# Performance work log

Hardware: AMD Instinct MI355X
Metric: run time of the kernel (lower is better)

Reference implementation:

```python
import jax, jax.numpy as jnp
import numpy as np

L, N, E = 2048, 2, 1024
H = 16
INNER = 1024
D = INNER // H  # head dim = 64
SCALE = D ** -0.5


def setup_inputs() -> dict:
    key = jax.random.key(0)
    k1, k2, k3, k4, k5 = jax.random.split(key, 5)
    return {
        "query": jax.random.normal(k1, (L, N, E), dtype=jnp.float32),
        "qkv_proj": jax.random.normal(k2, (3 * INNER, E), dtype=jnp.float32) * 0.02,
        "qkv_bias": jax.random.normal(k3, (3 * INNER,), dtype=jnp.float32) * 0.02,
        "out_proj": jax.random.normal(k4, (E, INNER), dtype=jnp.float32) * 0.02,
        "out_bias": jax.random.normal(k5, (E,), dtype=jnp.float32) * 0.02,
    }


def reference(query, qkv_proj, qkv_bias, out_proj, out_bias):
    # qkv combined projection: [L, N, 3*inner]
    qkv = jnp.einsum('lne,fe->lnf', query, qkv_proj) + qkv_bias
    # torch code views [L, N, 3*inner] as [L, N, inner, 3]: q/k/v interleaved
    qkv = qkv.reshape(L, N, INNER, 3)
    q, k, v = qkv[..., 0], qkv[..., 1], qkv[..., 2]  # each [L, N, inner]
    # [L, N*H, D] -> [N*H, L, D] (batched over batch*heads)
    q = q.reshape(L, N * H, D).transpose(1, 0, 2)
    k = k.reshape(L, N * H, D).transpose(1, 0, 2)
    v = v.reshape(L, N * H, D).transpose(1, 0, 2)
    # scores [N*H, L, L], scaled
    attn = SCALE * jnp.einsum('bld,bmd->blm', q, k)
    attn = jax.nn.softmax(attn, axis=-1)  # dropout_p = 0.0
    out = jnp.einsum('blm,bmd->bld', attn, v)  # [N*H, L, D]
    out = out.transpose(1, 0, 2).reshape(L, N, INNER)
    # output projection + bias
    return jnp.einsum('lni,ei->lne', out, out_proj) + out_bias
```

## Files before the change

### kernel.cpp

```cpp
#include <hip/hip_runtime.h>
#include <stdint.h>

#define SCALE 0.125f
#define LOG2E 1.44269504088896340736f
#define QK_SCALE (SCALE * LOG2E)

typedef __bf16 bf16x8 __attribute__((ext_vector_type(8)));
typedef float f32x4 __attribute__((ext_vector_type(4)));
typedef float f32x16 __attribute__((ext_vector_type(16)));
typedef unsigned u32x4 __attribute__((ext_vector_type(4)));

__device__ __forceinline__ ushort f2bf(float x) {
    union { float f; unsigned u; } v; v.f = x;
    unsigned r = v.u + 0x7FFFu + ((v.u >> 16) & 1u);
    return (ushort)(r >> 16);
}

__device__ __forceinline__ void gld_lds16(const void* g, void* l) {
    __builtin_amdgcn_global_load_lds(
        reinterpret_cast<const unsigned __attribute__((address_space(1)))*>(
            reinterpret_cast<uintptr_t>(g)),
        reinterpret_cast<unsigned __attribute__((address_space(3)))*>(
            (unsigned)reinterpret_cast<uintptr_t>(l)),
        16, 0, 0);
}

__global__ __launch_bounds__(256) void cast_fused(const float* __restrict__ s0,
                                                  const float* __restrict__ s1,
                                                  const float* __restrict__ s2,
                                                  ushort* __restrict__ d0,
                                                  ushort* __restrict__ d1,
                                                  ushort* __restrict__ d2) {
    int i = blockIdx.x * 256 + threadIdx.x;
    const float* src; ushort* dst; int idx;
    if (i < 1048576)            { src = s0; dst = d0; idx = i; }
    else if (i < 1048576 + 786432) { src = s1; dst = d1; idx = i - 1048576; }
    else                        { src = s2; dst = d2; idx = i - (1048576 + 786432); }
    float4 v = ((const float4*)src)[idx];
    ushort4 o;
    o.x = f2bf(v.x); o.y = f2bf(v.y); o.z = f2bf(v.z); o.w = f2bf(v.w);
    ((ushort4*)dst)[idx] = o;
}

__global__ __launch_bounds__(256, 3) void gemm_qkv(
    const ushort* __restrict__ A, const ushort* __restrict__ B,
    const float* __restrict__ bias,
    ushort* __restrict__ qh, ushort* __restrict__ kh, ushort* __restrict__ vT)
{
    __shared__ ushort As[128][64];
    __shared__ ushort Bs[128][64];
    const int tid = threadIdx.x;
    const int lane = tid & 63, wave = tid >> 6;
    const int wr = (wave >> 1) * 64, wc = (wave & 1) * 64;
    const int lr = lane & 15, lg = lane >> 4;
    const int swz = (lr & 7) << 4;
    const int sl = lane >> 3;
    const int scol = ((lane & 7) ^ sl) * 8;
    const int rowBase = blockIdx.y * 128;
    const int which = blockIdx.x >> 3;
    const int i0 = (blockIdx.x & 7) * 128;

    f32x4 acc[4][4] = {};
    for (int k0 = 0; k0 < 1024; k0 += 64) {
        __syncthreads();
        int s0 = wave * 4;
#pragma unroll
        for (int i = 0; i < 4; ++i) {
            int s = s0 + i;
            int r = s * 8 + sl;
            gld_lds16(A + (size_t)(rowBase + r) * 1024 + k0 + scol, &As[s * 8][0]);
            gld_lds16(B + (size_t)(3 * (i0 + r) + which) * 1024 + k0 + scol, &Bs[s * 8][0]);
        }
        __syncthreads();
#pragma unroll
        for (int kk = 0; kk < 2; ++kk) {
            bf16x8 af[4], bfr[4];
#pragma unroll
            for (int m = 0; m < 4; ++m)
                af[m] = *(const bf16x8*)((const char*)As + (wr + m * 16 + lr) * 128 + ((kk * 64 + lg * 16) ^ swz));
#pragma unroll
            for (int n = 0; n < 4; ++n)
                bfr[n] = *(const bf16x8*)((const char*)Bs + (wc + n * 16 + lr) * 128 + ((kk * 64 + lg * 16) ^ swz));
#pragma unroll
            for (int m = 0; m < 4; ++m)
#pragma unroll
                for (int n = 0; n < 4; ++n)
                    acc[m][n] = __builtin_amdgcn_mfma_f32_16x16x32_bf16(af[m], bfr[n], acc[m][n], 0, 0, 0);
        }
    }
#pragma unroll
    for (int n = 0; n < 4; ++n) {
        int i = i0 + wc + n * 16 + lr;
        float bv = bias[3 * i + which];
        int h = i >> 6, d = i & 63;
#pragma unroll
        for (int m = 0; m < 4; ++m) {
#pragma unroll
            for (int j = 0; j < 4; ++j) {
                int row = rowBase + wr + m * 16 + lg * 4 + j;
                int l = row >> 1, nb = row & 1;
                int bh = nb * 16 + h;
                float v = acc[m][n][j] + bv;
                if (which == 0)      qh[((size_t)bh * 2048 + l) * 64 + d] = f2bf(v * QK_SCALE);
                else if (which == 1) kh[((size_t)bh * 2048 + l) * 64 + d] = f2bf(v);
                else {
                    int lp = (l & ~12) | ((l & 4) << 1) | ((l & 8) >> 1);
                    vT[((size_t)bh * 64 + d) * 2048 + lp] = f2bf(v);
                }
            }
        }
    }
}

__global__ __launch_bounds__(512, 4) void attn_kernel(
    const ushort* __restrict__ qh, const ushort* __restrict__ kh,
    const ushort* __restrict__ vT, ushort* __restrict__ attn_out)
{
    __shared__ __align__(16) char smem[65536];
    const int tid = threadIdx.x, lane = tid & 63, wave = tid >> 6;
    const int group = wave >> 2, sub = wave & 3;
    const int l31 = lane & 31, hi = lane >> 5;
    const int swz = (lane & 7) << 4;
    const int b = blockIdx.y;
    const int qBase = blockIdx.x * 128;
    const int qrow = qBase + sub * 32 + l31;
    const int sl = lane >> 3;
    const int scol = ((lane & 7) ^ sl) * 8;
    const size_t kBase = (size_t)b * 2048;
    const size_t vBase = (size_t)b * 64;
    char* Kg = smem + group * 16384;
    char* Vg = smem + 32768 + group * 16384;
    const int tg0 = group * 16;

    bf16x8 qf[4];
#pragma unroll
    for (int kk = 0; kk < 4; ++kk)
        qf[kk] = *(const bf16x8*)(qh + (kBase + qrow) * 64 + kk * 16 + hi * 8);

    f32x16 ot[2] = {};
    float mrun = -1e30f, lsum = 0.f;

    {
        int s0 = sub * 2;
#pragma unroll
        for (int i = 0; i < 2; ++i) {
            int s = s0 + i;
            gld_lds16(kh + (kBase + tg0 * 64 + s * 8 + sl) * 64 + scol, Kg + s * 1024);
            gld_lds16(vT + (vBase + s * 8 + sl) * 2048 + tg0 * 64 + scol, Vg + s * 1024);
        }
    }
    __syncthreads();

    int buf = 0;
    for (int t = 0; t < 16; ++t) {
        if (t < 15) {
            int s0 = sub * 2;
#pragma unroll
            for (int i = 0; i < 2; ++i) {
                int s = s0 + i;
                gld_lds16(kh + (kBase + (tg0 + t + 1) * 64 + s * 8 + sl) * 64 + scol,
                          Kg + (buf ^ 1) * 8192 + s * 1024);
                gld_lds16(vT + (vBase + s * 8 + sl) * 2048 + (tg0 + t + 1) * 64 + scol,
                          Vg + (buf ^ 1) * 8192 + s * 1024);
            }
        }
        const char* kb = Kg + buf * 8192;
        const char* vb = Vg + buf * 8192;

        f32x16 sc[2] = {};
        __builtin_amdgcn_s_setprio(1);
#pragma unroll
        for (int blk = 0; blk < 2; ++blk) {
#pragma unroll
            for (int kk = 0; kk < 4; ++kk) {
                bf16x8 kf = *(const bf16x8*)(kb + (blk * 32 + l31) * 128 + ((kk * 32 + hi * 16) ^ swz));
                sc[blk] = __builtin_amdgcn_mfma_f32_32x32x16_bf16(kf, qf[kk], sc[blk], 0, 0, 0);
            }
        }
        __builtin_amdgcn_s_setprio(0);

        float tm[8];
#pragma unroll
        for (int i = 0; i < 8; ++i)
            tm[i] = fmaxf(fmaxf(sc[0][i], sc[0][i + 8]), fmaxf(sc[1][i], sc[1][i + 8]));
#pragma unroll
        for (int i = 0; i < 4; ++i)
            tm[i] = fmaxf(tm[i], tm[i + 4]);
        float mx = fmaxf(fmaxf(tm[0], tm[2]), fmaxf(tm[1], tm[3]));
        mx = fmaxf(mx, __shfl_xor(mx, 32));
        if (!__all(mx - mrun <= 8.0f)) {
            float mnew = fmaxf(mrun, mx);
            float alpha = __builtin_amdgcn_exp2f(mrun - mnew);
            mrun = mnew;
            lsum *= alpha;
#pragma unroll
            for (int blk = 0; blk < 2; ++blk)
#pragma unroll
                for (int r = 0; r < 16; ++r)
                    ot[blk][r] *= alpha;
        }
#pragma unroll
        for (int blk = 0; blk < 2; ++blk)
#pragma unroll
            for (int r = 0; r < 16; ++r)
                sc[blk][r] = __builtin_amdgcn_exp2f(sc[blk][r] - mrun);
        float ts[8];
#pragma unroll
        for (int i = 0; i < 8; ++i)
            ts[i] = (sc[0][i] + sc[0][i + 8]) + (sc[1][i] + sc[1][i + 8]);
#pragma unroll
        for (int i = 0; i < 4; ++i)
            ts[i] += ts[i + 4];
        float rs = (ts[0] + ts[2]) + (ts[1] + ts[3]);
        rs += __shfl_xor(rs, 32);
        lsum += rs;

        __builtin_amdgcn_s_setprio(1);
#pragma unroll
        for (int g = 0; g < 4; ++g) {
            const int blk = g >> 1;
            const int base = (g & 1) * 8;
            unsigned A0, A1, B0, B1;
            asm("v_cvt_pk_bf16_f32 %0, %1, %2" : "=v"(A0) : "v"(sc[blk][base + 0]), "v"(sc[blk][base + 1]));
            asm("v_cvt_pk_bf16_f32 %0, %1, %2" : "=v"(A1) : "v"(sc[blk][base + 2]), "v"(sc[blk][base + 3]));
            asm("v_cvt_pk_bf16_f32 %0, %1, %2" : "=v"(B0) : "v"(sc[blk][base + 4]), "v"(sc[blk][base + 5]));
            asm("v_cvt_pk_bf16_f32 %0, %1, %2" : "=v"(B1) : "v"(sc[blk][base + 6]), "v"(sc[blk][base + 7]));
            u32x4 pw; pw[0] = A0; pw[1] = A1; pw[2] = B0; pw[3] = B1;
            bf16x8 pb = __builtin_bit_cast(bf16x8, pw);
#pragma unroll
            for (int dblk = 0; dblk < 2; ++dblk) {
                bf16x8 vf = *(const bf16x8*)(vb + (dblk * 32 + l31) * 128 + ((g * 32 + hi * 16) ^ swz));
                ot[dblk] = __builtin_amdgcn_mfma_f32_32x32x16_bf16(vf, pb, ot[dblk], 0, 0, 0);
            }
        }
        __builtin_amdgcn_s_setprio(0);
        __syncthreads();
        buf ^= 1;
    }

    float* MO = (float*)smem;
    float* ML = (float*)(smem + 34816);
    if (group) {
        float* mo = MO + (sub * 32 + l31) * 68;
#pragma unroll
        for (int dblk = 0; dblk < 2; ++dblk)
#pragma unroll
            for (int m = 0; m < 4; ++m) {
                float4 st;
                st.x = ot[dblk][4 * m + 0]; st.y = ot[dblk][4 * m + 1];
                st.z = ot[dblk][4 * m + 2]; st.w = ot[dblk][4 * m + 3];
                *(float4*)(mo + dblk * 32 + m * 8 + hi * 4) = st;
            }
        if (!hi) {
            ML[(sub * 32 + l31) * 2 + 0] = mrun;
            ML[(sub * 32 + l31) * 2 + 1] = lsum;
        }
    }
    __syncthreads();
    if (!group) {
        float m1 = ML[(sub * 32 + l31) * 2 + 0];
        float l1 = ML[(sub * 32 + l31) * 2 + 1];
        float mmax = fmaxf(mrun, m1);
        float w0 = __builtin_amdgcn_exp2f(mrun - mmax);
        float w1 = __builtin_amdgcn_exp2f(m1 - mmax);
        float inv = __builtin_amdgcn_rcpf(lsum * w0 + l1 * w1);
        const float* mo = MO + (sub * 32 + l31) * 68;
        const int nb = b >> 4, h = b & 15;
        const size_t row = (size_t)qrow * 2 + nb;
#pragma unroll
        for (int dblk = 0; dblk < 2; ++dblk) {
#pragma unroll
            for (int m = 0; m < 4; ++m) {
                float4 oo = *(const float4*)(mo + dblk * 32 + m * 8 + hi * 4);
                float a0 = (ot[dblk][4 * m + 0] * w0 + oo.x * w1) * inv;
                float a1 = (ot[dblk][4 * m + 1] * w0 + oo.y * w1) * inv;
                float a2 = (ot[dblk][4 * m + 2] * w0 + oo.z * w1) * inv;
                float a3 = (ot[dblk][4 * m + 3] * w0 + oo.w * w1) * inv;
                unsigned w0p, w1p;
                asm("v_cvt_pk_bf16_f32 %0, %1, %2" : "=v"(w0p) : "v"(a0), "v"(a1));
                asm("v_cvt_pk_bf16_f32 %0, %1, %2" : "=v"(w1p) : "v"(a2), "v"(a3));
                uint2 st; st.x = w0p; st.y = w1p;
                *(uint2*)(attn_out + row * 1024 + h * 64 + dblk * 32 + m * 8 + hi * 4) = st;
            }
        }
    }
}

__global__ __launch_bounds__(256, 3) void gemm_out(
    const ushort* __restrict__ A, const ushort* __restrict__ B,
    const float* __restrict__ bias, float* __restrict__ out)
{
    __shared__ ushort As[128][64];
    __shared__ ushort Bs[64][64];
    const int tid = threadIdx.x;
    const int lane = tid & 63, wave = tid >> 6;
    const int wr = (wave >> 1) * 64, wc = (wave & 1) * 32;
    const int lr = lane & 15, lg = lane >> 4;
    const int swz = (lr & 7) << 4;
    const int sl = lane >> 3;
    const int scol = ((lane & 7) ^ sl) * 8;
    const int rowBase = blockIdx.y * 128, colBase = blockIdx.x * 64;

    f32x4 acc[4][2] = {};
    for (int k0 = 0; k0 < 1024; k0 += 64) {
        __syncthreads();
#pragma unroll
        for (int i = 0; i < 6; ++i) {
            int s = wave * 6 + i;
            if (s < 16)
                gld_lds16(A + (size_t)(rowBase + s * 8 + sl) * 1024 + k0 + scol, &As[s * 8][0]);
            else
                gld_lds16(B + (size_t)(colBase + (s - 16) * 8 + sl) * 1024 + k0 + scol, &Bs[(s - 16) * 8][0]);
        }
        __syncthreads();
#pragma unroll
        for (int kk = 0; kk < 2; ++kk) {
            bf16x8 af[4], bfr[2];
#pragma unroll
            for (int m = 0; m < 4; ++m)
                af[m] = *(const bf16x8*)((const char*)As + (wr + m * 16 + lr) * 128 + ((kk * 64 + lg * 16) ^ swz));
#pragma unroll
            for (int n = 0; n < 2; ++n)
                bfr[n] = *(const bf16x8*)((const char*)Bs + (wc + n * 16 + lr) * 128 + ((kk * 64 + lg * 16) ^ swz));
#pragma unroll
            for (int m = 0; m < 4; ++m)
#pragma unroll
                for (int n = 0; n < 2; ++n)
                    acc[m][n] = __builtin_amdgcn_mfma_f32_16x16x32_bf16(af[m], bfr[n], acc[m][n], 0, 0, 0);
        }
    }
#pragma unroll
    for (int n = 0; n < 2; ++n) {
        int e = colBase + wc + n * 16 + lr;
        float bv = bias[e];
#pragma unroll
        for (int m = 0; m < 4; ++m) {
#pragma unroll
            for (int j = 0; j < 4; ++j) {
                int row = rowBase + wr + m * 16 + lg * 4 + j;
                out[(size_t)row * 1024 + e] = acc[m][n][j] + bv;
            }
        }
    }
}

extern "C" void kernel_launch(void* const* d_in, const int* in_sizes, int n_in,
                              void* d_out, int out_size, void* d_ws, size_t ws_size,
                              hipStream_t stream) {
    const float* query    = (const float*)d_in[0];
    const float* qkv_proj = (const float*)d_in[1];
    const float* qkv_bias = (const float*)d_in[2];
    const float* out_proj = (const float*)d_in[3];
    const float* out_bias = (const float*)d_in[4];
    float* out = (float*)d_out;

    char* ws = (char*)d_ws;
    ushort* qbf      = (ushort*)ws;
    ushort* wqkv     = (ushort*)(ws + (8ull << 20));
    ushort* wout     = (ushort*)(ws + (14ull << 20));
    ushort* qh       = (ushort*)(ws + (16ull << 20));
    ushort* kh       = (ushort*)(ws + (24ull << 20));
    ushort* vT       = (ushort*)(ws + (32ull << 20));
    ushort* attn_out = (ushort*)(ws + (40ull << 20));

    cast_fused<<<8192, 256, 0, stream>>>(query, qkv_proj, out_proj, qbf, wqkv, wout);
    gemm_qkv<<<dim3(24, 32), 256, 0, stream>>>(qbf, wqkv, qkv_bias, qh, kh, vT);
    attn_kernel<<<dim3(16, 32), 512, 0, stream>>>(qh, kh, vT, attn_out);
    gemm_out<<<dim3(16, 32), 256, 0, stream>>>(attn_out, wout, out_bias, out);
}
```

Measured before the change: 120.2 us.

## Halve attention KV tile to 32 keys to cut LDS and raise occupancy

Shrinks the per-iteration key/value tile from 64 to 32 keys, halving LDS usage (64KB to 35KB) and the score registers per wave. Launch bounds move from 4 to 8 blocks per CU, and the V tile gets a new swizzle for its 64-byte rows. Each wave now makes 32 loop iterations instead of 16. The aim is more resident waves to hide latency, at the cost of more barriers, more softmax max/sum bookkeeping per key, and less MFMA work between synchronisations.

Result: slower. 235.1 us (+95.6%).

```diff
diff --git a/kernel.cpp b/kernel.cpp
--- a/kernel.cpp
+++ b/kernel.cpp
@@ -112,25 +112,28 @@
     }
 }
 
-__global__ __launch_bounds__(512, 4) void attn_kernel(
+__global__ __launch_bounds__(512, 8) void attn_kernel(
     const ushort* __restrict__ qh, const ushort* __restrict__ kh,
     const ushort* __restrict__ vT, ushort* __restrict__ attn_out)
 {
-    __shared__ __align__(16) char smem[65536];
+    __shared__ __align__(16) char smem[35840];
     const int tid = threadIdx.x, lane = tid & 63, wave = tid >> 6;
     const int group = wave >> 2, sub = wave & 3;
     const int l31 = lane & 31, hi = lane >> 5;
     const int swz = (lane & 7) << 4;
+    const int vphi = (l31 >> 1) & 3;
     const int b = blockIdx.y;
     const int qBase = blockIdx.x * 128;
     const int qrow = qBase + sub * 32 + l31;
-    const int sl = lane >> 3;
-    const int scol = ((lane & 7) ^ sl) * 8;
+    const int ksl = lane >> 3;
+    const int kcol = ((lane & 7) ^ ksl) * 8;
+    const int vdr = lane >> 2;
+    const int vcol = ((lane & 3) ^ ((lane >> 3) & 3)) * 8;
     const size_t kBase = (size_t)b * 2048;
     const size_t vBase = (size_t)b * 64;
-    char* Kg = smem + group * 16384;
-    char* Vg = smem + 32768 + group * 16384;
-    const int tg0 = group * 16;
+    char* Kg = smem + group * 8192;
+    char* Vg = smem + 16384 + group * 8192;
+    const int tg0 = group * 32;
 
     bf16x8 qf[4];
 #pragma unroll
@@ -140,53 +143,39 @@
     f32x16 ot[2] = {};
     float mrun = -1e30f, lsum = 0.f;
 
-    {
-        int s0 = sub * 2;
-#pragma unroll
-        for (int i = 0; i < 2; ++i) {
-            int s = s0 + i;
-            gld_lds16(kh + (kBase + tg0 * 64 + s * 8 + sl) * 64 + scol, Kg + s * 1024);
-            gld_lds16(vT + (vBase + s * 8 + sl) * 2048 + tg0 * 64 + scol, Vg + s * 1024);
-        }
-    }
+    gld_lds16(kh + (kBase + tg0 * 32 + sub * 8 + ksl) * 64 + kcol, Kg + sub * 1024);
+    gld_lds16(vT + (vBase + sub * 16 + vdr) * 2048 + tg0 * 32 + vcol, Vg + sub * 1024);
     __syncthreads();
 
     int buf = 0;
-    for (int t = 0; t < 16; ++t) {
-        if (t < 15) {
-            int s0 = sub * 2;
-#pragma unroll
-            for (int i = 0; i < 2; ++i) {
-                int s = s0 + i;
-                gld_lds16(kh + (kBase + (tg0 + t + 1) * 64 + s * 8 + sl) * 64 + scol,
-                          Kg + (buf ^ 1) * 8192 + s * 1024);
-                gld_lds16(vT + (vBase + s * 8 + sl) * 2048 + (tg0 + t + 1) * 64 + scol,
-                          Vg + (buf ^ 1) * 8192 + s * 1024);
-            }
-        }
-        const char* kb = Kg + buf * 8192;
-        const char* vb = Vg + buf * 8192;
-
-        f32x16 sc[2] = {};
+    for (int t = 0; t < 32; ++t) {
+        if (t < 31) {
+            int tt = tg0 + t + 1;
+            gld_lds16(kh + (kBase + tt * 32 + sub * 8 + ksl) * 64 + kcol,
+                      Kg + (buf ^ 1) * 4096 + sub * 1024);
+            gld_lds16(vT + (vBase + sub * 16 + vdr) * 2048 + tt * 32 + vcol,
+                      Vg + (buf ^ 1) * 4096 + sub * 1024);
+        }
+        const char* kb = Kg + buf * 4096;
+        const char* vb = Vg + buf * 4096;
+
+        f32x16 sc = {};
         __builtin_amdgcn_s_setprio(1);
 #pragma unroll
-        for (int blk = 0; blk < 2; ++blk) {
-#pragma unroll
-            for (int kk = 0; kk < 4; ++kk) {
-                bf16x8 kf = *(const bf16x8*)(kb + (blk * 32 + l31) * 128 + ((kk * 32 + hi * 16) ^ swz));
-                sc[blk] = __builtin_amdgcn_mfma_f32_32x32x16_bf16(kf, qf[kk], sc[blk], 0, 0, 0);
-            }
+        for (int kk = 0; kk < 4; ++kk) {
+            bf16x8 kf = *(const bf16x8*)(kb + l31 * 128 + ((kk * 32 + hi * 16) ^ swz));
+            sc = __builtin_amdgcn_mfma_f32_32x32x16_bf16(kf, qf[kk], sc, 0, 0, 0);
         }
         __builtin_amdgcn_s_setprio(0);
 
         float tm[8];
 #pragma unroll
         for (int i = 0; i < 8; ++i)
-            tm[i] = fmaxf(fmaxf(sc[0][i], sc[0][i + 8]), fmaxf(sc[1][i], sc[1][i + 8]));
+            tm[i] = fmaxf(sc[i], sc[i + 8]);
 #pragma unroll
         for (int i = 0; i < 4; ++i)
             tm[i] = fmaxf(tm[i], tm[i + 4]);
-        float mx = fmaxf(fmaxf(tm[0], tm[2]), fmaxf(tm[1], tm[3]));
+        float mx = fmaxf(fmaxf(tm[0], tm[1]), fmaxf(tm[2], tm[3]));
         mx = fmaxf(mx, __shfl_xor(mx, 32));
         if (!__all(mx - mrun <= 8.0f)) {
             float mnew = fmaxf(mrun, mx);
@@ -200,36 +189,33 @@
                     ot[blk][r] *= alpha;
         }
 #pragma unroll
-        for (int blk = 0; blk < 2; ++blk)
-#pragma unroll
-            for (int r = 0; r < 16; ++r)
-                sc[blk][r] = __builtin_amdgcn_exp2f(sc[blk][r] - mrun);
+        for (int r = 0; r < 16; ++r)
+            sc[r] = __builtin_amdgcn_exp2f(sc[r] - mrun);
         float ts[8];
 #pragma unroll
         for (int i = 0; i < 8; ++i)
-            ts[i] = (sc[0][i] + sc[0][i + 8]) + (sc[1][i] + sc[1][i + 8]);
+            ts[i] = sc[i] + sc[i + 8];
 #pragma unroll
         for (int i = 0; i < 4; ++i)
             ts[i] += ts[i + 4];
-        float rs = (ts[0] + ts[2]) + (ts[1] + ts[3]);
+        float rs = (ts[0] + ts[1]) + (ts[2] + ts[3]);
         rs += __shfl_xor(rs, 32);
         lsum += rs;
 
         __builtin_amdgcn_s_setprio(1);
 #pragma unroll
-        for (int g = 0; g < 4; ++g) {
-            const int blk = g >> 1;
-            const int base = (g & 1) * 8;
+        for (int g = 0; g < 2; ++g) {
+            const int base = g * 8;
             unsigned A0, A1, B0, B1;
-            asm("v_cvt_pk_bf16_f32 %0, %1, %2" : "=v"(A0) : "v"(sc[blk][base + 0]), "v"(sc[blk][base + 1]));
-            asm("v_cvt_pk_bf16_f32 %0, %1, %2" : "=v"(A1) : "v"(sc[blk][base + 2]), "v"(sc[blk][base + 3]));
-            asm("v_cvt_pk_bf16_f32 %0, %1, %2" : "=v"(B0) : "v"(sc[blk][base + 4]), "v"(sc[blk][base + 5]));
-            asm("v_cvt_pk_bf16_f32 %0, %1, %2" : "=v"(B1) : "v"(sc[blk][base + 6]), "v"(sc[blk][base + 7]));
+            asm("v_cvt_pk_bf16_f32 %0, %1, %2" : "=v"(A0) : "v"(sc[base + 0]), "v"(sc[base + 1]));
+            asm("v_cvt_pk_bf16_f32 %0, %1, %2" : "=v"(A1) : "v"(sc[base + 2]), "v"(sc[base + 3]));
+            asm("v_cvt_pk_bf16_f32 %0, %1, %2" : "=v"(B0) : "v"(sc[base + 4]), "v"(sc[base + 5]));
+            asm("v_cvt_pk_bf16_f32 %0, %1, %2" : "=v"(B1) : "v"(sc[base + 6]), "v"(sc[base + 7]));
             u32x4 pw; pw[0] = A0; pw[1] = A1; pw[2] = B0; pw[3] = B1;
             bf16x8 pb = __builtin_bit_cast(bf16x8, pw);
 #pragma unroll
             for (int dblk = 0; dblk < 2; ++dblk) {
-                bf16x8 vf = *(const bf16x8*)(vb + (dblk * 32 + l31) * 128 + ((g * 32 + hi * 16) ^ swz));
+                bf16x8 vf = *(const bf16x8*)(vb + (dblk * 32 + l31) * 64 + (((g * 2 + hi) ^ vphi) << 4));
                 ot[dblk] = __builtin_amdgcn_mfma_f32_32x32x16_bf16(vf, pb, ot[dblk], 0, 0, 0);
             }
         }
```
